# Kernel tuning notes

Hardware: AMD Instinct MI355X
Metric: run time of the kernel (lower is better)

## Reference

```python
import jax, jax.numpy as jnp
import numpy as np

NQ = 20
P_MAX = 480 * 640 - 1  # hardcoded clamp in original module


def make_quantizer_params(nq=NQ, mn=0.0, mx=1.0):
    # Replicates APLoss.__init__ conv1d weight/bias initialization.
    a = (nq - 1) / (mx - mn)
    w = np.concatenate([-a * np.ones(nq), a * np.ones(nq)]).astype(np.float32)
    b = np.concatenate([a * mn + np.arange(nq, 0, -1),
                        np.arange(2 - nq, 2, 1) - a * mn]).astype(np.float32)
    w[0] = w[-1] = 0.0
    b[0] = b[-1] = 1.0
    return jnp.asarray(w), jnp.asarray(b)


def setup_inputs() -> dict:
    key = jax.random.key(0)
    k1, k2, k3, k4, k5 = jax.random.split(key, 5)
    P, D, N, NEG = 307200, 64, 20000, 80
    qw, qb = make_quantizer_params()
    return {
        "descriptors1": jax.random.normal(k1, (1, P, D), dtype=jnp.float32),
        "descriptors2": jax.random.normal(k2, (1, P, D), dtype=jnp.float32),
        "qw": qw,
        "qb": qb,
        "matches_1": jax.random.randint(k3, (N,), 0, P),
        "matches_2": jax.random.randint(k4, (N,), 0, P),
        "offsets": jax.random.randint(k5, (NEG,), 0, 640),
    }


def reference(descriptors1, descriptors2, qw, qb, matches_1, matches_2, offsets):
    nq = qw.shape[0] // 2
    d1 = descriptors1[0]  # (P, D)
    d2 = descriptors2[0]  # (P, D)

    # negative indices: offset positive matches, clamp to valid pixel range
    non_m2 = jnp.clip(matches_2[:, None] + offsets[None, :], 0, P_MAX)  # (N, NEG)

    a1 = d1[matches_1]                                  # (N, D)
    pos = jnp.sum(a1 * d2[matches_2], axis=-1)          # (N,)
    neg = jnp.einsum('nd,nmd->nm', a1, d2[non_m2])      # (N, NEG)

    scores = jnp.concatenate([pos[:, None], neg], axis=1)   # (N, M), M = 1+NEG
    label = jnp.zeros_like(scores).at[:, 0].set(1.0)         # (N, M)

    # soft quantizer: 1x1 conv == per-bin affine; min of two halves, relu
    x = scores[:, None, :]                                   # (N, 1, M)
    q = jnp.minimum(qw[:nq, None] * x + qb[:nq, None],
                    qw[nq:, None] * x + qb[nq:, None])
    q = jnp.maximum(q, 0.0)                                  # (N, nq, M)

    nbs = q.sum(axis=-1)                                     # (N, nq)
    rec = (q * label[:, None, :]).sum(axis=-1)               # (N, nq)
    prec = jnp.cumsum(rec, axis=-1) / (1e-16 + jnp.cumsum(nbs, axis=-1))
    rec = rec / rec.sum(axis=-1, keepdims=True)
    ap = (prec * rec).sum(axis=-1)                           # (N,)
    return (1.0 - ap).mean()
```

## Files before the change

### kernel.cpp

```cpp
#include <hip/hip_runtime.h>

#define DIM 64


__global__ __launch_bounds__(256) void k_hist(const int* __restrict__ m2,
                                              int* __restrict__ cnt, int N) {
    const int i = blockIdx.x * 256 + threadIdx.x;
    if (i < N) atomicAdd(&cnt[m2[i] >> 7], 1);
}

__global__ __launch_bounds__(256) void k_scan(int* __restrict__ cnt, int nbuck) {
    __shared__ int s[256];
    const int tid  = threadIdx.x;
    const int base = tid * 10;
    int loc[10];
    int sum = 0;
    #pragma unroll
    for (int u = 0; u < 10; ++u) {
        const int idx = base + u;
        const int v = (idx < nbuck) ? cnt[idx] : 0;
        loc[u] = sum;
        sum += v;
    }
    s[tid] = sum;
    __syncthreads();
    for (int off = 1; off < 256; off <<= 1) {
        const int v = (tid >= off) ? s[tid - off] : 0;
        __syncthreads();
        s[tid] += v;
        __syncthreads();
    }
    const int excl = (tid > 0) ? s[tid - 1] : 0;
    #pragma unroll
    for (int u = 0; u < 10; ++u) {
        const int idx = base + u;
        if (idx < nbuck) cnt[idx] = excl + loc[u];
    }
}

__global__ __launch_bounds__(256) void k_scatter(const int* __restrict__ m1,
                                                 const int* __restrict__ m2,
                                                 int* __restrict__ cnt,
                                                 int* __restrict__ i1s,
                                                 int* __restrict__ i2s, int N) {
    const int i = blockIdx.x * 256 + threadIdx.x;
    if (i < N) {
        const int v2  = m2[i];
        const int pos = atomicAdd(&cnt[v2 >> 7], 1);
        i1s[pos] = m1[i];
        i2s[pos] = v2;
    }
}

__global__ __launch_bounds__(256) void pixel_ap_main(
    const float* __restrict__ d1, const float* __restrict__ d2,
    const float* __restrict__ qw, const float* __restrict__ qb,
    const int* __restrict__ offs,
    const int* __restrict__ i1s, const int* __restrict__ i2s,
    float* __restrict__ partial, int P, int NEG, int NQ2, int N)
{
    const int tid = threadIdx.x;
    const int nq  = NQ2 >> 1;
    const int M   = NEG + 1;

    __shared__ float s_scores[2][96];

    const int b    = blockIdx.x;
    const int per  = gridDim.x >> 3;
    const int pr   = (b & 7) * per + (b >> 3);
    const int posA = 2 * pr;
    const int posB = posA + 1;
    if (posA >= N) return;
    const bool hasB = (posB < N);

    const int i1A = i1s[posA];
    const int i2A = i2s[posA];
    const int i1B = hasB ? i1s[posB] : i1A;
    const int i2B = hasB ? i2s[posB] : i2A;

    const int g  = tid >> 3;
    const int sl = tid & 7;

    const float* aA = d1 + (size_t)i1A * DIM + 8 * sl;
    const float* aB = d1 + (size_t)i1B * DIM + 8 * sl;
    const float4 a0A = ((const float4*)aA)[0];
    const float4 a1A = ((const float4*)aA)[1];
    const float4 a0B = ((const float4*)aB)[0];
    const float4 a1B = ((const float4*)aB)[1];

    int rA[3], rB[3];
    #pragma unroll
    for (int t = 0; t < 3; ++t) {
        const int j = g + 32 * t;
        if (j < M) {
            const int o = (j == 0) ? 0 : offs[j - 1];
            rA[t] = (j == 0) ? i2A : min(i2A + o, P - 1);
            rB[t] = (j == 0) ? i2B : min(i2B + o, P - 1);
        }
    }

    float4 b0A[3], b1A[3], b0B[3], b1B[3];
    #pragma unroll
    for (int t = 0; t < 3; ++t) {
        const int j = g + 32 * t;
        if (j < M) {
            const float* pA = d2 + (size_t)rA[t] * DIM + 8 * sl;
            b0A[t] = ((const float4*)pA)[0];
            b1A[t] = ((const float4*)pA)[1];
            const float* pB = d2 + (size_t)rB[t] * DIM + 8 * sl;
            b0B[t] = ((const float4*)pB)[0];
            b1B[t] = ((const float4*)pB)[1];
        }
    }
    #pragma unroll
    for (int t = 0; t < 3; ++t) {
        const int j = g + 32 * t;
        if (j < M) {
            float sA = b0A[t].x * a0A.x + b0A[t].y * a0A.y + b0A[t].z * a0A.z + b0A[t].w * a0A.w
                     + b1A[t].x * a1A.x + b1A[t].y * a1A.y + b1A[t].z * a1A.z + b1A[t].w * a1A.w;
            float sB = b0B[t].x * a0B.x + b0B[t].y * a0B.y + b0B[t].z * a0B.z + b0B[t].w * a0B.w
                     + b1B[t].x * a1B.x + b1B[t].y * a1B.y + b1B[t].z * a1B.z + b1B[t].w * a1B.w;
            sA += __shfl_xor(sA, 1);
            sA += __shfl_xor(sA, 2);
            sA += __shfl_xor(sA, 4);
            sB += __shfl_xor(sB, 1);
            sB += __shfl_xor(sB, 2);
            sB += __shfl_xor(sB, 4);
            if (sl == 0) {
                s_scores[0][j] = sA;
                s_scores[1][j] = sB;
            }
        }
    }
    __syncthreads();
    const int w = tid >> 6;
    if (w >= 2) return;
    if (w == 1 && !hasB) return;
    const int lane = tid & 63;

    const float a_scale = qw[nq];
    const float amn     = qb[nq - 1] - 1.0f;
    const float ulim    = (float)(nq - 1);

    const float xp = s_scores[w][0];
    const float up = fminf(fmaxf(a_scale * xp - amn, 0.0f), ulim);
    const float ip = floorf(up);
    const float fp = up - ip;

    float n1 = 0.0f, n2 = 0.0f;
    {
        const float x  = s_scores[w][lane];
        const float u  = fminf(fmaxf(a_scale * x - amn, 0.0f), ulim);
        const float fi = floorf(u);
        const float f  = u - fi;
        n2 += (fi >= ip)        ? 1.0f : ((fi == ip - 1.0f) ? f : 0.0f);
        n1 += (fi >= ip + 1.0f) ? 1.0f : ((fi == ip)        ? f : 0.0f);
    }
    if (lane + 64 < M) {
        const float x  = s_scores[w][lane + 64];
        const float u  = fminf(fmaxf(a_scale * x - amn, 0.0f), ulim);
        const float fi = floorf(u);
        const float f  = u - fi;
        n2 += (fi >= ip)        ? 1.0f : ((fi == ip - 1.0f) ? f : 0.0f);
        n1 += (fi >= ip + 1.0f) ? 1.0f : ((fi == ip)        ? f : 0.0f);
    }
    #pragma unroll
    for (int off = 32; off >= 1; off >>= 1) {
        n1 += __shfl_xor(n1, off);
        n2 += __shfl_xor(n2, off);
    }
    if (lane == 0) {
        const float ap = fp * fp / (1e-16f + n1) + (1.0f - fp) / (1e-16f + n2);
        partial[posA + w] = 1.0f - ap;
    }
}

__global__ __launch_bounds__(1024) void k_reduce(const float* __restrict__ partial,
                                                 float* __restrict__ out, int N)
{
    float s = 0.0f;
    for (int i = threadIdx.x; i < N; i += 1024) s += partial[i];
    #pragma unroll
    for (int off = 32; off >= 1; off >>= 1) s += __shfl_xor(s, off);
    __shared__ float sw[16];
    if ((threadIdx.x & 63) == 0) sw[threadIdx.x >> 6] = s;
    __syncthreads();
    if (threadIdx.x == 0) {
        float t = 0.0f;
        #pragma unroll
        for (int w = 0; w < 16; ++w) t += sw[w];
        out[0] = t / (float)N;
    }
}

extern "C" void kernel_launch(void* const* d_in, const int* in_sizes, int n_in,
                              void* d_out, int out_size, void* d_ws, size_t ws_size,
                              hipStream_t stream) {
    const float* d1   = (const float*)d_in[0];
    const float* d2   = (const float*)d_in[1];
    const float* qw   = (const float*)d_in[2];
    const float* qb   = (const float*)d_in[3];
    const int*   m1   = (const int*)d_in[4];
    const int*   m2   = (const int*)d_in[5];
    const int*   offs = (const int*)d_in[6];

    const int N     = in_sizes[4];
    const int P     = in_sizes[0] / DIM;
    const int NEG   = in_sizes[6];
    const int NQ2   = in_sizes[2];
    const int nbuck = (P + 127) >> 7;

    int*   cnt     = (int*)d_ws;
    int*   i1s     = cnt + nbuck;
    int*   i2s     = i1s + N;
    float* partial = (float*)(i2s + N);

    const int nblk = (N + 255) / 256;

    hipMemsetAsync(cnt, 0, (size_t)nbuck * sizeof(int), stream);
    k_hist   <<<nblk, 256, 0, stream>>>(m2, cnt, N);
    k_scan   <<<1, 256, 0, stream>>>(cnt, nbuck);
    k_scatter<<<nblk, 256, 0, stream>>>(m1, m2, cnt, i1s, i2s, N);

    const int npair = (N + 1) / 2;
    const int per   = (npair + 7) / 8;
    pixel_ap_main<<<8 * per, 256, 0, stream>>>(d1, d2, qw, qb, offs, i1s, i2s,
                                               partial, P, NEG, NQ2, N);

    k_reduce<<<1, 1024, 0, stream>>>(partial, (float*)d_out, N);
}
```

Baseline: 198.2 us.

## Fuse sort, AP compute and reduction into one cooperative persistent kernel

Replaces the memset, histogram, scan, scatter, main and reduce launches with a single cooperative kernel that separates the phases with grid-wide syncs. Blocks loop persistently over match pairs, double-buffer the score tile in shared memory, and reduce per block before a final grid reduction. This removes several kernel launches and the launch gaps between them. In exchange it adds grid.sync overhead, and the persistent grid caps parallelism for the gather-heavy main phase. The old multi-kernel path is kept as a fallback if the cooperative launch fails.

```diff
diff --git a/kernel.cpp b/kernel.cpp
--- a/kernel.cpp
+++ b/kernel.cpp
@@ -1,7 +1,212 @@
 #include <hip/hip_runtime.h>
-
-#define DIM 64
-
+#include <hip/hip_cooperative_groups.h>
+
+namespace cg = cooperative_groups;
+
+#define DIM  64
+#define TPB  256
+
+__global__ __launch_bounds__(TPB, 4) void fused_ap(
+    const float* __restrict__ d1, const float* __restrict__ d2,
+    const float* __restrict__ qw, const float* __restrict__ qb,
+    const int* __restrict__ m1, const int* __restrict__ m2,
+    const int* __restrict__ offs,
+    int* __restrict__ cnt, int* __restrict__ i1s, int* __restrict__ i2s,
+    float* __restrict__ blocksum, float* __restrict__ out,
+    int P, int NEG, int NQ2, int N)
+{
+    cg::grid_group grid = cg::this_grid();
+
+    __shared__ int   s_scan[256];
+    __shared__ float s_scores[2][2][96];
+    __shared__ float s_red[4];
+
+    const int tid   = threadIdx.x;
+    const int b     = blockIdx.x;
+    const int nG    = gridDim.x;
+    const int gtid  = b * TPB + tid;
+    const int gstr  = nG * TPB;
+    const int nbuck = (P + 127) >> 7;
+
+    for (int i = gtid; i < nbuck; i += gstr) cnt[i] = 0;
+    __threadfence();
+    grid.sync();
+
+    for (int i = gtid; i < N; i += gstr) atomicAdd(&cnt[m2[i] >> 7], 1);
+    __threadfence();
+    grid.sync();
+
+    if (b == 0) {
+        const int base = tid * 10;
+        int loc[10];
+        int sum = 0;
+        #pragma unroll
+        for (int u = 0; u < 10; ++u) {
+            const int idx = base + u;
+            const int v = (idx < nbuck) ? cnt[idx] : 0;
+            loc[u] = sum;
+            sum += v;
+        }
+        s_scan[tid] = sum;
+        __syncthreads();
+        for (int off = 1; off < 256; off <<= 1) {
+            const int v = (tid >= off) ? s_scan[tid - off] : 0;
+            __syncthreads();
+            s_scan[tid] += v;
+            __syncthreads();
+        }
+        const int excl = (tid > 0) ? s_scan[tid - 1] : 0;
+        #pragma unroll
+        for (int u = 0; u < 10; ++u) {
+            const int idx = base + u;
+            if (idx < nbuck) cnt[idx] = excl + loc[u];
+        }
+    }
+    __threadfence();
+    grid.sync();
+
+    for (int i = gtid; i < N; i += gstr) {
+        const int v2  = m2[i];
+        const int pos = atomicAdd(&cnt[v2 >> 7], 1);
+        i1s[pos] = m1[i];
+        i2s[pos] = v2;
+    }
+    __threadfence();
+    grid.sync();
+
+    const int npair = (N + 1) >> 1;
+    const int per8  = (npair + 7) >> 3;
+    const int pbeg  = (b & 7) * per8;
+    const int pend  = (pbeg + per8 < npair) ? (pbeg + per8) : npair;
+    const int slots = nG >> 3;
+    const int g     = tid >> 3;
+    const int sl    = tid & 7;
+    const int w     = tid >> 6;
+    const int lane  = tid & 63;
+    const int M     = NEG + 1;
+    const int nq    = NQ2 >> 1;
+    const float a_scale = qw[nq];
+    const float amn     = qb[nq - 1] - 1.0f;
+    const float ulim    = (float)(nq - 1);
+
+    float acc = 0.0f;
+    int it = 0;
+    for (int pr = pbeg + (b >> 3); pr < pend; pr += slots, ++it) {
+        float (*sc)[96] = s_scores[it & 1];
+        const int posA = 2 * pr;
+        const int posB = posA + 1;
+        const bool hasB = (posB < N);
+        const int i1A = i1s[posA];
+        const int i2A = i2s[posA];
+        const int i1B = hasB ? i1s[posB] : i1A;
+        const int i2B = hasB ? i2s[posB] : i2A;
+
+        const float* aA = d1 + (size_t)i1A * DIM + 8 * sl;
+        const float* aB = d1 + (size_t)i1B * DIM + 8 * sl;
+        const float4 a0A = ((const float4*)aA)[0];
+        const float4 a1A = ((const float4*)aA)[1];
+        const float4 a0B = ((const float4*)aB)[0];
+        const float4 a1B = ((const float4*)aB)[1];
+
+        int rA[3], rB[3];
+        #pragma unroll
+        for (int t = 0; t < 3; ++t) {
+            const int j = g + 32 * t;
+            if (j < M) {
+                const int o = (j == 0) ? 0 : offs[j - 1];
+                rA[t] = (j == 0) ? i2A : min(i2A + o, P - 1);
+                rB[t] = (j == 0) ? i2B : min(i2B + o, P - 1);
+            }
+        }
+
+        float4 b0A[3], b1A[3], b0B[3], b1B[3];
+        #pragma unroll
+        for (int t = 0; t < 3; ++t) {
+            const int j = g + 32 * t;
+            if (j < M) {
+                const float* pA = d2 + (size_t)rA[t] * DIM + 8 * sl;
+                b0A[t] = ((const float4*)pA)[0];
+                b1A[t] = ((const float4*)pA)[1];
+                const float* pB = d2 + (size_t)rB[t] * DIM + 8 * sl;
+                b0B[t] = ((const float4*)pB)[0];
+                b1B[t] = ((const float4*)pB)[1];
+            }
+        }
+        #pragma unroll
+        for (int t = 0; t < 3; ++t) {
+            const int j = g + 32 * t;
+            if (j < M) {
+                float sA = b0A[t].x * a0A.x + b0A[t].y * a0A.y + b0A[t].z * a0A.z + b0A[t].w * a0A.w
+                         + b1A[t].x * a1A.x + b1A[t].y * a1A.y + b1A[t].z * a1A.z + b1A[t].w * a1A.w;
+                float sB = b0B[t].x * a0B.x + b0B[t].y * a0B.y + b0B[t].z * a0B.z + b0B[t].w * a0B.w
+                         + b1B[t].x * a1B.x + b1B[t].y * a1B.y + b1B[t].z * a1B.z + b1B[t].w * a1B.w;
+                sA += __shfl_xor(sA, 1);
+                sA += __shfl_xor(sA, 2);
+                sA += __shfl_xor(sA, 4);
+                sB += __shfl_xor(sB, 1);
+                sB += __shfl_xor(sB, 2);
+                sB += __shfl_xor(sB, 4);
+                if (sl == 0) {
+                    sc[0][j] = sA;
+                    sc[1][j] = sB;
+                }
+            }
+        }
+        __syncthreads();
+        if (w < 2 && (w == 0 || hasB)) {
+            const float xp = sc[w][0];
+            const float up = fminf(fmaxf(a_scale * xp - amn, 0.0f), ulim);
+            const float ip = floorf(up);
+            const float fp = up - ip;
+
+            float n1 = 0.0f, n2 = 0.0f;
+            {
+                const float x  = sc[w][lane];
+                const float u  = fminf(fmaxf(a_scale * x - amn, 0.0f), ulim);
+                const float fi = floorf(u);
+                const float f  = u - fi;
+                n2 += (fi >= ip)        ? 1.0f : ((fi == ip - 1.0f) ? f : 0.0f);
+                n1 += (fi >= ip + 1.0f) ? 1.0f : ((fi == ip)        ? f : 0.0f);
+            }
+            if (lane + 64 < M) {
+                const float x  = sc[w][lane + 64];
+                const float u  = fminf(fmaxf(a_scale * x - amn, 0.0f), ulim);
+                const float fi = floorf(u);
+                const float f  = u - fi;
+                n2 += (fi >= ip)        ? 1.0f : ((fi == ip - 1.0f) ? f : 0.0f);
+                n1 += (fi >= ip + 1.0f) ? 1.0f : ((fi == ip)        ? f : 0.0f);
+            }
+            #pragma unroll
+            for (int off = 32; off >= 1; off >>= 1) {
+                n1 += __shfl_xor(n1, off);
+                n2 += __shfl_xor(n2, off);
+            }
+            if (lane == 0) {
+                const float ap = fp * fp / (1e-16f + n1) + (1.0f - fp) / (1e-16f + n2);
+                acc += 1.0f - ap;
+            }
+        }
+    }
+
+    __syncthreads();
+    if (tid == 0)  s_red[0] = acc;
+    if (tid == 64) s_red[1] = acc;
+    __syncthreads();
+    if (tid == 0) blocksum[b] = s_red[0] + s_red[1];
+    __threadfence();
+    grid.sync();
+
+    if (b == 0) {
+        float s = 0.0f;
+        for (int i = tid; i < nG; i += TPB) s += blocksum[i];
+        #pragma unroll
+        for (int off = 32; off >= 1; off >>= 1) s += __shfl_xor(s, off);
+        __syncthreads();
+        if ((tid & 63) == 0) s_red[tid >> 6] = s;
+        __syncthreads();
+        if (tid == 0) out[0] = (s_red[0] + s_red[1] + s_red[2] + s_red[3]) / (float)N;
+    }
+}
 
 __global__ __launch_bounds__(256) void k_hist(const int* __restrict__ m2,
                                               int* __restrict__ cnt, int N) {
@@ -204,28 +409,59 @@
     const int*   m2   = (const int*)d_in[5];
     const int*   offs = (const int*)d_in[6];
 
-    const int N     = in_sizes[4];
-    const int P     = in_sizes[0] / DIM;
-    const int NEG   = in_sizes[6];
-    const int NQ2   = in_sizes[2];
+    int N   = in_sizes[4];
+    int P   = in_sizes[0] / DIM;
+    int NEG = in_sizes[6];
+    int NQ2 = in_sizes[2];
     const int nbuck = (P + 127) >> 7;
 
-    int*   cnt     = (int*)d_ws;
-    int*   i1s     = cnt + nbuck;
-    int*   i2s     = i1s + N;
-    float* partial = (float*)(i2s + N);
-
-    const int nblk = (N + 255) / 256;
-
-    hipMemsetAsync(cnt, 0, (size_t)nbuck * sizeof(int), stream);
-    k_hist   <<<nblk, 256, 0, stream>>>(m2, cnt, N);
-    k_scan   <<<1, 256, 0, stream>>>(cnt, nbuck);
-    k_scatter<<<nblk, 256, 0, stream>>>(m1, m2, cnt, i1s, i2s, N);
-
-    const int npair = (N + 1) / 2;
-    const int per   = (npair + 7) / 8;
-    pixel_ap_main<<<8 * per, 256, 0, stream>>>(d1, d2, qw, qb, offs, i1s, i2s,
-                                               partial, P, NEG, NQ2, N);
-
-    k_reduce<<<1, 1024, 0, stream>>>(partial, (float*)d_out, N);
-}
+    int*   cnt      = (int*)d_ws;
+    int*   i1s      = cnt + nbuck;
+    int*   i2s      = i1s + N;
+    float* blocksum = (float*)(i2s + N);
+    float* outp     = (float*)d_out;
+
+    static int s_grid = -2;
+    if (s_grid == -2) {
+        int blocksPerCU = 0;
+        hipError_t e1 = hipOccupancyMaxActiveBlocksPerMultiprocessor(
+            &blocksPerCU, fused_ap, TPB, 0);
+        int numCU = 0;
+        hipError_t e2 = hipDeviceGetAttribute(
+            &numCU, hipDeviceAttributeMultiprocessorCount, 0);
+        if (e1 == hipSuccess && e2 == hipSuccess && blocksPerCU > 0 && numCU > 0) {
+            int maxg = blocksPerCU * numCU;
+            if (maxg > 2048) maxg = 2048;
+            s_grid = (maxg / 8) * 8;
+            if (s_grid < 8) s_grid = -1;
+        } else {
+            s_grid = -1;
+        }
+    }
+
+    hipError_t err = hipErrorUnknown;
+    if (s_grid >= 8) {
+        void* args[] = { (void*)&d1, (void*)&d2, (void*)&qw, (void*)&qb,
+                         (void*)&m1, (void*)&m2, (void*)&offs,
+                         (void*)&cnt, (void*)&i1s, (void*)&i2s,
+                         (void*)&blocksum, (void*)&outp,
+                         (void*)&P, (void*)&NEG, (void*)&NQ2, (void*)&N };
+        err = hipLaunchCooperativeKernel(fused_ap, dim3(s_grid), dim3(TPB),
+                                         args, 0, stream);
+    }
+
+    if (err != hipSuccess) {
+        s_grid = -1;
+        const int nblk = (N + 255) / 256;
+        hipMemsetAsync(cnt, 0, (size_t)nbuck * sizeof(int), stream);
+        k_hist   <<<nblk, 256, 0, stream>>>(m2, cnt, N);
+        k_scan   <<<1, 256, 0, stream>>>(cnt, nbuck);
+        k_scatter<<<nblk, 256, 0, stream>>>(m1, m2, cnt, i1s, i2s, N);
+        const int npair = (N + 1) / 2;
+        const int per   = (npair + 7) / 8;
+        pixel_ap_main<<<8 * per, 256, 0, stream>>>(d1, d2, qw, qb, offs,
+                                                   i1s, i2s, blocksum,
+                                                   P, NEG, NQ2, N);
+        k_reduce<<<1, 1024, 0, stream>>>(blocksum, outp, N);
+    }
+}
```

Measured after the change: 643.1 us. 3.24x slower.

## Fuse bucket sort into one LDS kernel and fold final reduction into main kernel

Applied to the files above, without the earlier changes.

Replaces the memset, histogram, scan and scatter kernels with a single 1024-thread block that builds the bucket histogram in shared memory, scans it and scatters the match indices. The separate reduction kernel is removed: the main kernel atomically accumulates per-match losses into a global float, and the last block to finish, detected with a done counter, writes the mean. This cuts four kernel launches and their gaps. In exchange, sorting runs on a single workgroup, float atomics make the summation order nondeterministic, and every block now contends on one global accumulator.

```diff
diff --git a/kernel.cpp b/kernel.cpp
--- a/kernel.cpp
+++ b/kernel.cpp
@@ -2,51 +2,45 @@
 
 #define DIM 64
 
-
-__global__ __launch_bounds__(256) void k_hist(const int* __restrict__ m2,
-                                              int* __restrict__ cnt, int N) {
-    const int i = blockIdx.x * 256 + threadIdx.x;
-    if (i < N) atomicAdd(&cnt[m2[i] >> 7], 1);
-}
-
-__global__ __launch_bounds__(256) void k_scan(int* __restrict__ cnt, int nbuck) {
-    __shared__ int s[256];
-    const int tid  = threadIdx.x;
-    const int base = tid * 10;
-    int loc[10];
-    int sum = 0;
-    #pragma unroll
-    for (int u = 0; u < 10; ++u) {
-        const int idx = base + u;
-        const int v = (idx < nbuck) ? cnt[idx] : 0;
-        loc[u] = sum;
-        sum += v;
-    }
-    s[tid] = sum;
-    __syncthreads();
-    for (int off = 1; off < 256; off <<= 1) {
-        const int v = (tid >= off) ? s[tid - off] : 0;
+__global__ __launch_bounds__(1024) void k_sort(
+    const int* __restrict__ m1, const int* __restrict__ m2,
+    int* __restrict__ i1s, int* __restrict__ i2s,
+    float* __restrict__ acc, unsigned int* __restrict__ done,
+    int N, int nbuck, int shift)
+{
+    __shared__ int h[3072];
+    __shared__ int ssc[1024];
+    const int tid = threadIdx.x;
+
+    if (tid == 0) { acc[0] = 0.0f; done[0] = 0u; }
+    for (int i = tid; i < nbuck; i += 1024) h[i] = 0;
+    __syncthreads();
+
+    for (int i = tid; i < N; i += 1024) atomicAdd(&h[m2[i] >> shift], 1);
+    __syncthreads();
+
+    const int base = tid * 3;
+    int l0 = 0, l1 = 0, l2 = 0, sum = 0;
+    if (base + 0 < nbuck) { l0 = sum; sum += h[base + 0]; }
+    if (base + 1 < nbuck) { l1 = sum; sum += h[base + 1]; }
+    if (base + 2 < nbuck) { l2 = sum; sum += h[base + 2]; }
+    ssc[tid] = sum;
+    __syncthreads();
+    for (int off = 1; off < 1024; off <<= 1) {
+        const int v = (tid >= off) ? ssc[tid - off] : 0;
         __syncthreads();
-        s[tid] += v;
+        ssc[tid] += v;
         __syncthreads();
     }
-    const int excl = (tid > 0) ? s[tid - 1] : 0;
-    #pragma unroll
-    for (int u = 0; u < 10; ++u) {
-        const int idx = base + u;
-        if (idx < nbuck) cnt[idx] = excl + loc[u];
-    }
-}
-
-__global__ __launch_bounds__(256) void k_scatter(const int* __restrict__ m1,
-                                                 const int* __restrict__ m2,
-                                                 int* __restrict__ cnt,
-                                                 int* __restrict__ i1s,
-                                                 int* __restrict__ i2s, int N) {
-    const int i = blockIdx.x * 256 + threadIdx.x;
-    if (i < N) {
+    const int excl = (tid > 0) ? ssc[tid - 1] : 0;
+    if (base + 0 < nbuck) h[base + 0] = excl + l0;
+    if (base + 1 < nbuck) h[base + 1] = excl + l1;
+    if (base + 2 < nbuck) h[base + 2] = excl + l2;
+    __syncthreads();
+
+    for (int i = tid; i < N; i += 1024) {
         const int v2  = m2[i];
-        const int pos = atomicAdd(&cnt[v2 >> 7], 1);
+        const int pos = atomicAdd(&h[v2 >> shift], 1);
         i1s[pos] = m1[i];
         i2s[pos] = v2;
     }
@@ -57,7 +51,8 @@
     const float* __restrict__ qw, const float* __restrict__ qb,
     const int* __restrict__ offs,
     const int* __restrict__ i1s, const int* __restrict__ i2s,
-    float* __restrict__ partial, int P, int NEG, int NQ2, int N)
+    float* __restrict__ acc, unsigned int* __restrict__ done,
+    float* __restrict__ out, int P, int NEG, int NQ2, int N)
 {
     const int tid = threadIdx.x;
     const int nq  = NQ2 >> 1;
@@ -70,126 +65,120 @@
     const int pr   = (b & 7) * per + (b >> 3);
     const int posA = 2 * pr;
     const int posB = posA + 1;
-    if (posA >= N) return;
-    const bool hasB = (posB < N);
-
-    const int i1A = i1s[posA];
-    const int i2A = i2s[posA];
-    const int i1B = hasB ? i1s[posB] : i1A;
-    const int i2B = hasB ? i2s[posB] : i2A;
+    const bool active = (posA < N);
+    const bool hasB   = (posB < N);
 
     const int g  = tid >> 3;
     const int sl = tid & 7;
-
-    const float* aA = d1 + (size_t)i1A * DIM + 8 * sl;
-    const float* aB = d1 + (size_t)i1B * DIM + 8 * sl;
-    const float4 a0A = ((const float4*)aA)[0];
-    const float4 a1A = ((const float4*)aA)[1];
-    const float4 a0B = ((const float4*)aB)[0];
-    const float4 a1B = ((const float4*)aB)[1];
-
-    int rA[3], rB[3];
-    #pragma unroll
-    for (int t = 0; t < 3; ++t) {
-        const int j = g + 32 * t;
-        if (j < M) {
-            const int o = (j == 0) ? 0 : offs[j - 1];
-            rA[t] = (j == 0) ? i2A : min(i2A + o, P - 1);
-            rB[t] = (j == 0) ? i2B : min(i2B + o, P - 1);
-        }
-    }
-
-    float4 b0A[3], b1A[3], b0B[3], b1B[3];
-    #pragma unroll
-    for (int t = 0; t < 3; ++t) {
-        const int j = g + 32 * t;
-        if (j < M) {
-            const float* pA = d2 + (size_t)rA[t] * DIM + 8 * sl;
-            b0A[t] = ((const float4*)pA)[0];
-            b1A[t] = ((const float4*)pA)[1];
-            const float* pB = d2 + (size_t)rB[t] * DIM + 8 * sl;
-            b0B[t] = ((const float4*)pB)[0];
-            b1B[t] = ((const float4*)pB)[1];
-        }
-    }
-    #pragma unroll
-    for (int t = 0; t < 3; ++t) {
-        const int j = g + 32 * t;
-        if (j < M) {
-            float sA = b0A[t].x * a0A.x + b0A[t].y * a0A.y + b0A[t].z * a0A.z + b0A[t].w * a0A.w
-                     + b1A[t].x * a1A.x + b1A[t].y * a1A.y + b1A[t].z * a1A.z + b1A[t].w * a1A.w;
-            float sB = b0B[t].x * a0B.x + b0B[t].y * a0B.y + b0B[t].z * a0B.z + b0B[t].w * a0B.w
-                     + b1B[t].x * a1B.x + b1B[t].y * a1B.y + b1B[t].z * a1B.z + b1B[t].w * a1B.w;
-            sA += __shfl_xor(sA, 1);
-            sA += __shfl_xor(sA, 2);
-            sA += __shfl_xor(sA, 4);
-            sB += __shfl_xor(sB, 1);
-            sB += __shfl_xor(sB, 2);
-            sB += __shfl_xor(sB, 4);
-            if (sl == 0) {
-                s_scores[0][j] = sA;
-                s_scores[1][j] = sB;
+    const int w  = tid >> 6;
+    const int lane = tid & 63;
+
+    if (active) {
+        const int i1A = i1s[posA];
+        const int i2A = i2s[posA];
+        const int i1B = hasB ? i1s[posB] : i1A;
+        const int i2B = hasB ? i2s[posB] : i2A;
+
+        const float* aA = d1 + (size_t)i1A * DIM + 8 * sl;
+        const float* aB = d1 + (size_t)i1B * DIM + 8 * sl;
+        const float4 a0A = ((const float4*)aA)[0];
+        const float4 a1A = ((const float4*)aA)[1];
+        const float4 a0B = ((const float4*)aB)[0];
+        const float4 a1B = ((const float4*)aB)[1];
+
+        int rA[3], rB[3];
+        #pragma unroll
+        for (int t = 0; t < 3; ++t) {
+            const int j = g + 32 * t;
+            if (j < M) {
+                const int o = (j == 0) ? 0 : offs[j - 1];
+                rA[t] = (j == 0) ? i2A : min(i2A + o, P - 1);
+                rB[t] = (j == 0) ? i2B : min(i2B + o, P - 1);
             }
         }
-    }
-    __syncthreads();
-    const int w = tid >> 6;
-    if (w >= 2) return;
-    if (w == 1 && !hasB) return;
-    const int lane = tid & 63;
-
-    const float a_scale = qw[nq];
-    const float amn     = qb[nq - 1] - 1.0f;
-    const float ulim    = (float)(nq - 1);
-
-    const float xp = s_scores[w][0];
-    const float up = fminf(fmaxf(a_scale * xp - amn, 0.0f), ulim);
-    const float ip = floorf(up);
-    const float fp = up - ip;
-
-    float n1 = 0.0f, n2 = 0.0f;
-    {
-        const float x  = s_scores[w][lane];
-        const float u  = fminf(fmaxf(a_scale * x - amn, 0.0f), ulim);
-        const float fi = floorf(u);
-        const float f  = u - fi;
-        n2 += (fi >= ip)        ? 1.0f : ((fi == ip - 1.0f) ? f : 0.0f);
-        n1 += (fi >= ip + 1.0f) ? 1.0f : ((fi == ip)        ? f : 0.0f);
-    }
-    if (lane + 64 < M) {
-        const float x  = s_scores[w][lane + 64];
-        const float u  = fminf(fmaxf(a_scale * x - amn, 0.0f), ulim);
-        const float fi = floorf(u);
-        const float f  = u - fi;
-        n2 += (fi >= ip)        ? 1.0f : ((fi == ip - 1.0f) ? f : 0.0f);
-        n1 += (fi >= ip + 1.0f) ? 1.0f : ((fi == ip)        ? f : 0.0f);
-    }
-    #pragma unroll
-    for (int off = 32; off >= 1; off >>= 1) {
-        n1 += __shfl_xor(n1, off);
-        n2 += __shfl_xor(n2, off);
-    }
-    if (lane == 0) {
-        const float ap = fp * fp / (1e-16f + n1) + (1.0f - fp) / (1e-16f + n2);
-        partial[posA + w] = 1.0f - ap;
-    }
-}
-
-__global__ __launch_bounds__(1024) void k_reduce(const float* __restrict__ partial,
-                                                 float* __restrict__ out, int N)
-{
-    float s = 0.0f;
-    for (int i = threadIdx.x; i < N; i += 1024) s += partial[i];
-    #pragma unroll
-    for (int off = 32; off >= 1; off >>= 1) s += __shfl_xor(s, off);
-    __shared__ float sw[16];
-    if ((threadIdx.x & 63) == 0) sw[threadIdx.x >> 6] = s;
-    __syncthreads();
-    if (threadIdx.x == 0) {
-        float t = 0.0f;
-        #pragma unroll
-        for (int w = 0; w < 16; ++w) t += sw[w];
-        out[0] = t / (float)N;
+
+        float4 b0A[3], b1A[3], b0B[3], b1B[3];
+        #pragma unroll
+        for (int t = 0; t < 3; ++t) {
+            const int j = g + 32 * t;
+            if (j < M) {
+                const float* pA = d2 + (size_t)rA[t] * DIM + 8 * sl;
+                b0A[t] = ((const float4*)pA)[0];
+                b1A[t] = ((const float4*)pA)[1];
+                const float* pB = d2 + (size_t)rB[t] * DIM + 8 * sl;
+                b0B[t] = ((const float4*)pB)[0];
+                b1B[t] = ((const float4*)pB)[1];
+            }
+        }
+        #pragma unroll
+        for (int t = 0; t < 3; ++t) {
+            const int j = g + 32 * t;
+            if (j < M) {
+                float sA = b0A[t].x * a0A.x + b0A[t].y * a0A.y + b0A[t].z * a0A.z + b0A[t].w * a0A.w
+                         + b1A[t].x * a1A.x + b1A[t].y * a1A.y + b1A[t].z * a1A.z + b1A[t].w * a1A.w;
+                float sB = b0B[t].x * a0B.x + b0B[t].y * a0B.y + b0B[t].z * a0B.z + b0B[t].w * a0B.w
+                         + b1B[t].x * a1B.x + b1B[t].y * a1B.y + b1B[t].z * a1B.z + b1B[t].w * a1B.w;
+                sA += __shfl_xor(sA, 1);
+                sA += __shfl_xor(sA, 2);
+                sA += __shfl_xor(sA, 4);
+                sB += __shfl_xor(sB, 1);
+                sB += __shfl_xor(sB, 2);
+                sB += __shfl_xor(sB, 4);
+                if (sl == 0) {
+                    s_scores[0][j] = sA;
+                    s_scores[1][j] = sB;
+                }
+            }
+        }
+    }
+    __syncthreads();
+
+    if (active && w < 2 && (w == 0 || hasB)) {
+        const float a_scale = qw[nq];
+        const float amn     = qb[nq - 1] - 1.0f;
+        const float ulim    = (float)(nq - 1);
+
+        const float xp = s_scores[w][0];
+        const float up = fminf(fmaxf(a_scale * xp - amn, 0.0f), ulim);
+        const float ip = floorf(up);
+        const float fp = up - ip;
+
+        float n1 = 0.0f, n2 = 0.0f;
+        {
+            const float x  = s_scores[w][lane];
+            const float u  = fminf(fmaxf(a_scale * x - amn, 0.0f), ulim);
+            const float fi = floorf(u);
+            const float f  = u - fi;
+            n2 += (fi >= ip)        ? 1.0f : ((fi == ip - 1.0f) ? f : 0.0f);
+            n1 += (fi >= ip + 1.0f) ? 1.0f : ((fi == ip)        ? f : 0.0f);
+        }
+        if (lane + 64 < M) {
+            const float x  = s_scores[w][lane + 64];
+            const float u  = fminf(fmaxf(a_scale * x - amn, 0.0f), ulim);
+            const float fi = floorf(u);
+            const float f  = u - fi;
+            n2 += (fi >= ip)        ? 1.0f : ((fi == ip - 1.0f) ? f : 0.0f);
+            n1 += (fi >= ip + 1.0f) ? 1.0f : ((fi == ip)        ? f : 0.0f);
+        }
+        #pragma unroll
+        for (int off = 32; off >= 1; off >>= 1) {
+            n1 += __shfl_xor(n1, off);
+            n2 += __shfl_xor(n2, off);
+        }
+        if (lane == 0) {
+            const float ap = fp * fp / (1e-16f + n1) + (1.0f - fp) / (1e-16f + n2);
+            atomicAdd(acc, 1.0f - ap);
+        }
+    }
+
+    __syncthreads();
+    if (tid == 0) {
+        __threadfence();
+        const unsigned prev = atomicAdd(done, 1u);
+        if (prev == (unsigned)(gridDim.x - 1)) {
+            const float s = atomicAdd(acc, 0.0f);
+            out[0] = s / (float)N;
+        }
     }
 }
 
@@ -204,28 +193,25 @@
     const int*   m2   = (const int*)d_in[5];
     const int*   offs = (const int*)d_in[6];
 
-    const int N     = in_sizes[4];
-    const int P     = in_sizes[0] / DIM;
-    const int NEG   = in_sizes[6];
-    const int NQ2   = in_sizes[2];
-    const int nbuck = (P + 127) >> 7;
-
-    int*   cnt     = (int*)d_ws;
-    int*   i1s     = cnt + nbuck;
-    int*   i2s     = i1s + N;
-    float* partial = (float*)(i2s + N);
-
-    const int nblk = (N + 255) / 256;
-
-    hipMemsetAsync(cnt, 0, (size_t)nbuck * sizeof(int), stream);
-    k_hist   <<<nblk, 256, 0, stream>>>(m2, cnt, N);
-    k_scan   <<<1, 256, 0, stream>>>(cnt, nbuck);
-    k_scatter<<<nblk, 256, 0, stream>>>(m1, m2, cnt, i1s, i2s, N);
+    const int N   = in_sizes[4];
+    const int P   = in_sizes[0] / DIM;
+    const int NEG = in_sizes[6];
+    const int NQ2 = in_sizes[2];
+
+    int shift = 7;
+    while ((((P - 1) >> shift) + 1) > 3072) ++shift;
+    const int nbuck = ((P - 1) >> shift) + 1;
+
+    int*      i1s  = (int*)d_ws;
+    int*      i2s  = i1s + N;
+    float*    acc  = (float*)(i2s + N);
+    unsigned* done = (unsigned*)(acc + 1);
+
+    k_sort<<<1, 1024, 0, stream>>>(m1, m2, i1s, i2s, acc, done, N, nbuck, shift);
 
     const int npair = (N + 1) / 2;
     const int per   = (npair + 7) / 8;
     pixel_ap_main<<<8 * per, 256, 0, stream>>>(d1, d2, qw, qb, offs, i1s, i2s,
-                                               partial, P, NEG, NQ2, N);
-
-    k_reduce<<<1, 1024, 0, stream>>>(partial, (float*)d_out, N);
+                                               acc, done, (float*)d_out,
+                                               P, NEG, NQ2, N);
 }
```

After: 626.7 us. 216% more time.
